# Kernel optimization log

Measured on AMD Instinct MI355X. Metric: run time of the kernel, lower is better.

## Reference

```python
import jax, jax.numpy as jnp
import numpy as np

DIM = 1024
N_HEADS = 16
HEAD_DIM = DIM // N_HEADS


def setup_inputs() -> dict:
    key = jax.random.key(0)
    ks = jax.random.split(key, 5)
    scale = 1.0 / np.sqrt(DIM)
    x = jax.random.normal(ks[0], (2, 2048, DIM), dtype=jnp.float32)
    W_qkv = jax.random.normal(ks[1], (DIM, 3 * DIM), dtype=jnp.float32) * scale
    b_qkv = jax.random.normal(ks[2], (3 * DIM,), dtype=jnp.float32) * 0.01
    W_proj = jax.random.normal(ks[3], (DIM, DIM), dtype=jnp.float32) * scale
    b_proj = jax.random.normal(ks[4], (DIM,), dtype=jnp.float32) * 0.01
    return {"x": x, "W_qkv": W_qkv, "b_qkv": b_qkv, "W_proj": W_proj, "b_proj": b_proj}


def reference(x, W_qkv, b_qkv, W_proj, b_proj):
    B, T, C = x.shape
    qkv = x @ W_qkv + b_qkv  # [B,T,3C]
    q, k, v = jnp.split(qkv, 3, axis=2)
    # [B,T,C] -> [B,H,T,Dh]
    def heads(y):
        return y.reshape(B, T, N_HEADS, HEAD_DIM).transpose(0, 2, 1, 3)
    q, k, v = heads(q), heads(k), heads(v)
    inv_sqrt_dh = 1.0 / jnp.sqrt(jnp.asarray(HEAD_DIM, dtype=x.dtype))
    attn = jnp.einsum('bhqd,bhkd->bhqk', q, k) * inv_sqrt_dh
    attn = jax.nn.softmax(attn, axis=-1)
    out = jnp.einsum('bhqk,bhkd->bhqd', attn, v)
    out = out.transpose(0, 2, 1, 3).reshape(B, T, C)
    return out @ W_proj + b_proj
```

## Files before the change

kernel.cpp:

```cpp
#include <hip/hip_runtime.h>
#include <hip/hip_bf16.h>
#include <math.h>

using bf16 = __hip_bfloat16;

typedef __bf16 bf16x8 __attribute__((ext_vector_type(8)));
typedef __bf16 bf16x4 __attribute__((ext_vector_type(4)));
typedef float  f32x4  __attribute__((ext_vector_type(4)));
typedef float  f32x16 __attribute__((ext_vector_type(16)));

constexpr int Bb = 2;
constexpr int Ts = 2048;
constexpr int Cc = 1024;
constexpr int Hh = 16;
constexpr int Dh = 64;
constexpr int Mm = Bb * Ts;
constexpr int Nqkv = 3 * Cc;
constexpr int BHTD = Bb * Hh * Ts * Dh;

__device__ __forceinline__
void gll16(const __bf16* g, __bf16* l)
{
    __builtin_amdgcn_global_load_lds(
        (const __attribute__((address_space(1))) unsigned int*)g,
        (__attribute__((address_space(3))) unsigned int*)l,
        16, 0, 0);
}

__global__ __launch_bounds__(256)
void prep_all(const float* __restrict__ x, __bf16* __restrict__ Xb,
              const float* __restrict__ Wq, __bf16* __restrict__ Wqt,
              const float* __restrict__ Wp, __bf16* __restrict__ Wpt)
{
    __shared__ __bf16 tl[64][72];
    const int bid = blockIdx.x;
    const int t = threadIdx.x;

    if (bid < 4096) {
        int i = (bid * 256 + t) * 4;
        float4 v = *(const float4*)(x + i);
        bf16x4 o = { (__bf16)v.x, (__bf16)v.y, (__bf16)v.z, (__bf16)v.w };
        *(bf16x4*)(Xb + i) = o;
        return;
    }
    const float* W; __bf16* Wt; int cols, bx, by;
    if (bid < 4096 + 768) {
        W = Wq; Wt = Wqt; cols = Nqkv;
        bx = (bid - 4096) % 48; by = (bid - 4096) / 48;
    } else {
        W = Wp; Wt = Wpt; cols = Cc;
        bx = (bid - 4864) % 16; by = (bid - 4864) / 16;
    }
    const int c0 = bx * 64;
    const int r0 = by * 64;
    #pragma unroll
    for (int i = 0; i < 4; i++) {
        int e = t + 256 * i;
        int r = e >> 4, c4 = (e & 15) * 4;
        float4 v = *(const float4*)(W + (r0 + r) * cols + c0 + c4);
        bf16x4 o = { (__bf16)v.x, (__bf16)v.y, (__bf16)v.z, (__bf16)v.w };
        *(bf16x4*)&tl[r][c4] = o;
    }
    __syncthreads();
    #pragma unroll
    for (int i = 0; i < 4; i++) {
        int e = t + 256 * i;
        int n = e >> 4, k4 = (e & 15) * 4;
        bf16x4 o = { tl[k4][n], tl[k4 + 1][n], tl[k4 + 2][n], tl[k4 + 3][n] };
        *(bf16x4*)(Wt + (c0 + n) * 1024 + r0 + k4) = o;
    }
}

template<int BM>
__device__ __forceinline__
void gemm_core(const __bf16* __restrict__ A, const __bf16* __restrict__ Bt,
               int m0, int n0, int wm, int wn, int quad, int l16, int t,
               f32x4 (&acc)[4][4])
{
    __shared__ __bf16 Al[BM][32];
    __shared__ __bf16 Bl[128][32];

    constexpr int MT = BM / 32;
    const int wave = t >> 6;
    const int lane = t & 63;
    const int srow = lane >> 2;
    const int scol = (lane & 3) * 8;

    const __bf16* Ag = A  + (size_t)(m0 + wave * 16 + srow) * 1024 + scol;
    const __bf16* Bg = Bt + (size_t)(n0 + wave * 16 + srow) * 1024 + scol;
    __bf16* Al_lo = &Al[wave * 16][0];
    __bf16* Bl_lo = &Bl[wave * 16][0];
    __bf16* Bl_hi = &Bl[64 + wave * 16][0];

    for (int k0 = 0; k0 < 1024; k0 += 32) {
        gll16(Ag + k0, Al_lo);
        if constexpr (BM == 128) {
            __bf16* Al_hi = &Al[64 + wave * 16][0];
            gll16(Ag + k0 + 64 * 1024, Al_hi);
        }
        gll16(Bg + k0,             Bl_lo);
        gll16(Bg + k0 + 64 * 1024, Bl_hi);
        __syncthreads();
        bf16x8 af[MT], bfr[4];
        #pragma unroll
        for (int mt = 0; mt < MT; mt++)
            af[mt] = *(const bf16x8*)&Al[wm * (BM / 2) + mt * 16 + l16][quad * 8];
        #pragma unroll
        for (int nt = 0; nt < 4; nt++)
            bfr[nt] = *(const bf16x8*)&Bl[wn * 64 + nt * 16 + l16][quad * 8];
        #pragma unroll
        for (int mt = 0; mt < MT; mt++)
            #pragma unroll
            for (int nt = 0; nt < 4; nt++)
                acc[mt][nt] = __builtin_amdgcn_mfma_f32_16x16x32_bf16(
                    af[mt], bfr[nt], acc[mt][nt], 0, 0, 0);
        __syncthreads();
    }
}

__global__ __launch_bounds__(256)
void qkv_mfma(const __bf16* __restrict__ A, const __bf16* __restrict__ Bt,
              const float* __restrict__ bias, __bf16* __restrict__ qkv)
{
    __shared__ __bf16 ebuf[4][64][72];

    const int t    = threadIdx.x;
    const int wave = t >> 6;
    const int lane = t & 63;
    const int quad = lane >> 4;
    const int l16  = lane & 15;
    const int wm   = wave >> 1, wn = wave & 1;
    const int n0 = blockIdx.x * 128;
    const int m0 = blockIdx.y * 128;

    f32x4 acc[4][4];
    #pragma unroll
    for (int i = 0; i < 4; i++)
        #pragma unroll
        for (int j = 0; j < 4; j++)
            acc[i][j] = f32x4{0.f, 0.f, 0.f, 0.f};

    gemm_core<128>(A, Bt, m0, n0, wm, wn, quad, l16, t, acc);

    const int nw0 = n0 + wn * 64;
    const int which = nw0 >> 10;
    const int h = (nw0 & 1023) >> 6;

    if (which == 2) {
        #pragma unroll
        for (int nt = 0; nt < 4; nt++) {
            int d = nt * 16 + l16;
            float bs = bias[nw0 + nt * 16 + l16];
            #pragma unroll
            for (int mt = 0; mt < 4; mt++) {
                int m = m0 + wm * 64 + mt * 16 + quad * 4;
                int b = m >> 11;
                int tt = m & 2047;
                bf16x4 o = { (__bf16)(acc[mt][nt][0] + bs),
                             (__bf16)(acc[mt][nt][1] + bs),
                             (__bf16)(acc[mt][nt][2] + bs),
                             (__bf16)(acc[mt][nt][3] + bs) };
                *(bf16x4*)&qkv[2 * (size_t)BHTD +
                               (((size_t)(b * 16 + h) * 64 + d) * 2048 + tt)] = o;
            }
        }
    } else {
        #pragma unroll
        for (int nt = 0; nt < 4; nt++) {
            float bs = bias[nw0 + nt * 16 + l16];
            #pragma unroll
            for (int mt = 0; mt < 4; mt++)
                #pragma unroll
                for (int r = 0; r < 4; r++)
                    ebuf[wave][mt * 16 + quad * 4 + r][nt * 16 + l16] =
                        (__bf16)(acc[mt][nt][r] + bs);
        }
        int m = m0 + wm * 64 + lane;
        int b = m >> 11;
        int tt = m & 2047;
        __bf16* dst = &qkv[which * (size_t)BHTD +
                           (((size_t)(b * 16 + h) * 2048 + tt) * 64)];
        #pragma unroll
        for (int c = 0; c < 8; c++)
            *(bf16x8*)(dst + c * 8) = *(const bf16x8*)&ebuf[wave][lane][c * 8];
    }
}

__global__ __launch_bounds__(256)
void proj_mfma(const __bf16* __restrict__ A, const __bf16* __restrict__ Bt,
               const float* __restrict__ bias, float* __restrict__ out)
{
    const int t    = threadIdx.x;
    const int wave = t >> 6;
    const int lane = t & 63;
    const int quad = lane >> 4;
    const int l16  = lane & 15;
    const int wm   = wave >> 1, wn = wave & 1;
    const int n0 = blockIdx.x * 128;
    const int m0 = blockIdx.y * 64;

    f32x4 acc[4][4];
    #pragma unroll
    for (int i = 0; i < 4; i++)
        #pragma unroll
        for (int j = 0; j < 4; j++)
            acc[i][j] = f32x4{0.f, 0.f, 0.f, 0.f};

    gemm_core<64>(A, Bt, m0, n0, wm, wn, quad, l16, t, acc);

    #pragma unroll
    for (int nt = 0; nt < 4; nt++) {
        int n = n0 + wn * 64 + nt * 16 + l16;
        float bs = bias[n];
        #pragma unroll
        for (int mt = 0; mt < 2; mt++) {
            #pragma unroll
            for (int r = 0; r < 4; r++) {
                int m = m0 + wm * 32 + mt * 16 + quad * 4 + r;
                out[m * 1024 + n] = acc[mt][nt][r] + bs;
            }
        }
    }
}

__global__ __launch_bounds__(512, 2)
void attn_mfma(const __bf16* __restrict__ Q, const __bf16* __restrict__ K,
               const __bf16* __restrict__ VT, __bf16* __restrict__ O)
{
    __shared__ __bf16 sK[2][3][64 * 64];
    __shared__ __bf16 sV[2][3][64 * 64];
    __shared__ float  slsum[4][2][64];

    const int t    = threadIdx.x;
    const int wave = t >> 6;
    const int lane = t & 63;
    const int qg   = wave & 3;
    const int kh   = wave >> 2;
    const int c    = lane & 31;
    const int hi   = lane >> 5;
    const int hx   = hi * 16;
    const int sw   = (c & 7) << 4;

    const int blk = blockIdx.x;
    const int bh  = blk & 31;
    const int qc  = blk >> 5;
    const int q0  = qc * 256 + qg * 64;

    const __bf16* Qp = Q  + ((size_t)bh * Ts + q0) * Dh;
    const __bf16* Kp = K  + (size_t)bh * Ts * Dh;
    const __bf16* Vp = VT + (size_t)bh * Dh * Ts;

    const float qscale = 0.125f * 1.44269504088896f;
    bf16x8 qf[2][4];
    #pragma unroll
    for (int qs = 0; qs < 2; qs++)
        #pragma unroll
        for (int ds = 0; ds < 4; ds++) {
            bf16x8 v = *(const bf16x8*)(Qp + (qs * 32 + c) * Dh + ds * 16 + hi * 8);
            #pragma unroll
            for (int i = 0; i < 8; i++) v[i] = (__bf16)(qscale * (float)v[i]);
            qf[qs][ds] = v;
        }

    f32x16 accO[2][2];
    #pragma unroll
    for (int qs = 0; qs < 2; qs++)
        #pragma unroll
        for (int dt = 0; dt < 2; dt++)
            #pragma unroll
            for (int i = 0; i < 16; i++) accO[qs][dt][i] = 0.f;
    float lsum[2] = {0.f, 0.f};

    const f32x16 z16 = {0.f, 0.f, 0.f, 0.f, 0.f, 0.f, 0.f, 0.f,
                        0.f, 0.f, 0.f, 0.f, 0.f, 0.f, 0.f, 0.f};

    const int r0 = qg * 8 + (lane >> 3);
    const int s8 = ((lane & 7) ^ (r0 & 7)) * 8;
    const __bf16* kg0 = Kp + (size_t)(kh * 1024 + r0) * Dh + s8;
    const __bf16* kg1 = kg0 + 32 * Dh;
    const __bf16* vg0 = Vp + (size_t)r0 * Ts + kh * 1024 + s8;
    const __bf16* vg1 = vg0 + (size_t)32 * Ts;

    gll16(kg0, &sK[kh][0][qg * 512]);
    gll16(kg1, &sK[kh][0][2048 + qg * 512]);
    gll16(vg0, &sV[kh][0][qg * 512]);
    gll16(vg1, &sV[kh][0][2048 + qg * 512]);

    for (int j = 0; j < 16; j++) {
        const int p = j % 3;
        if (j < 15) {
            const int pn = (j + 1) % 3;
            gll16(kg0 + (j + 1) * 4096, &sK[kh][pn][qg * 512]);
            gll16(kg1 + (j + 1) * 4096, &sK[kh][pn][2048 + qg * 512]);
            gll16(vg0 + (j + 1) * 64,   &sV[kh][pn][qg * 512]);
            gll16(vg1 + (j + 1) * 64,   &sV[kh][pn][2048 + qg * 512]);
            asm volatile("s_waitcnt vmcnt(4)" ::: "memory");
        } else {
            asm volatile("s_waitcnt vmcnt(0)" ::: "memory");
        }
        __builtin_amdgcn_s_barrier();
        __builtin_amdgcn_sched_barrier(0);

        const char* kb = (const char*)&sK[kh][p][0];
        const char* vb = (const char*)&sV[kh][p][0];

        bf16x8 kf[2][4];
        #pragma unroll
        for (int kt = 0; kt < 2; kt++) {
            const char* rbase = kb + (kt * 32 + c) * 128;
            #pragma unroll
            for (int ds = 0; ds < 4; ds++)
                kf[kt][ds] = *(const bf16x8*)(rbase + ((ds * 32 + hx) ^ sw));
        }

        f32x16 st[2][2];
        __builtin_amdgcn_s_setprio(1);
        #pragma unroll
        for (int kt = 0; kt < 2; kt++)
            #pragma unroll
            for (int qs = 0; qs < 2; qs++)
                st[qs][kt] = __builtin_amdgcn_mfma_f32_32x32x16_bf16(
                    kf[kt][0], qf[qs][0], z16, 0, 0, 0);
        #pragma unroll
        for (int ds = 1; ds < 4; ds++)
            #pragma unroll
            for (int kt = 0; kt < 2; kt++)
                #pragma unroll
                for (int qs = 0; qs < 2; qs++)
                    st[qs][kt] = __builtin_amdgcn_mfma_f32_32x32x16_bf16(
                        kf[kt][ds], qf[qs][ds], st[qs][kt], 0, 0, 0);
        __builtin_amdgcn_s_setprio(0);

        bf16x8 pa[2][4];
        #pragma unroll
        for (int qs = 0; qs < 2; qs++) {
            unsigned pk[2][8];
            #pragma unroll
            for (int kt = 0; kt < 2; kt++) {
                float sum0 = 0.f, sum1 = 0.f;
                #pragma unroll
                for (int r = 0; r < 16; r++) {
                    float pv = __builtin_amdgcn_exp2f(st[qs][kt][r]);
                    st[qs][kt][r] = pv;
                    if (r & 1) sum1 += pv; else sum0 += pv;
                }
                lsum[qs] += sum0 + sum1;
                #pragma unroll
                for (int r2 = 0; r2 < 8; r2++) {
                    unsigned d;
                    asm("v_cvt_pk_bf16_f32 %0, %1, %2"
                        : "=v"(d)
                        : "v"(st[qs][kt][2 * r2]), "v"(st[qs][kt][2 * r2 + 1]));
                    pk[kt][r2] = d;
                }
            }
            #pragma unroll
            for (int s = 0; s < 4; s++) {
                const int kt = s >> 1, r4 = (s & 1) * 4;
                unsigned x0 = pk[kt][r4 + 0], y0 = pk[kt][r4 + 2];
                unsigned x1 = pk[kt][r4 + 1], y1 = pk[kt][r4 + 3];
                asm("v_permlane32_swap_b32 %0, %1" : "+v"(x0), "+v"(y0));
                asm("v_permlane32_swap_b32 %0, %1" : "+v"(x1), "+v"(y1));
                union { unsigned u[4]; bf16x8 b; } pu;
                pu.u[0] = x0; pu.u[1] = x1; pu.u[2] = y0; pu.u[3] = y1;
                pa[qs][s] = pu.b;
            }
        }

        __builtin_amdgcn_s_setprio(1);
        #pragma unroll
        for (int s = 0; s < 4; s++)
            #pragma unroll
            for (int dt = 0; dt < 2; dt++) {
                bf16x8 vf = *(const bf16x8*)(vb + (dt * 32 + c) * 128 +
                                             ((s * 32 + hx) ^ sw));
                #pragma unroll
                for (int qs = 0; qs < 2; qs++)
                    accO[qs][dt] = __builtin_amdgcn_mfma_f32_32x32x16_bf16(
                        pa[qs][s], vf, accO[qs][dt], 0, 0, 0);
            }
        __builtin_amdgcn_s_setprio(0);
    }

    __syncthreads();

    float* pb = (qg < 2) ? (float*)&sK[0][0][0] + qg * 4096
                         : (float*)&sV[0][0][0] + (qg - 2) * 4096;
    if (kh == 1) {
        #pragma unroll
        for (int qs = 0; qs < 2; qs++) {
            #pragma unroll
            for (int dt = 0; dt < 2; dt++)
                #pragma unroll
                for (int r = 0; r < 16; r++)
                    pb[((qs * 2 + dt) << 10) + (r << 6) + lane] = accO[qs][dt][r];
            slsum[qg][qs][lane] = lsum[qs];
        }
    }
    __syncthreads();
    if (kh == 0) {
        #pragma unroll
        for (int qs = 0; qs < 2; qs++) {
            #pragma unroll
            for (int dt = 0; dt < 2; dt++)
                #pragma unroll
                for (int r = 0; r < 16; r++)
                    accO[qs][dt][r] += pb[((qs * 2 + dt) << 10) + (r << 6) + lane];
            lsum[qs] += slsum[qg][qs][lane];
        }

        const int b = bh >> 4, h = bh & 15;
        #pragma unroll
        for (int qs = 0; qs < 2; qs++) {
            float l = lsum[qs] + __shfl_xor(lsum[qs], 32);
            float linv = 1.f / l;
            #pragma unroll
            for (int r = 0; r < 16; r++) {
                const int qrow = (r & 3) + 8 * (r >> 2) + 4 * hi;
                float inv = __shfl(linv, qrow);
                __bf16* Op = O + ((size_t)(b * Ts + q0 + qs * 32 + qrow)) * Cc +
                             h * 64 + c;
                Op[0]  = (__bf16)(accO[qs][0][r] * inv);
                Op[32] = (__bf16)(accO[qs][1][r] * inv);
            }
        }
    }
}

extern "C" void kernel_launch(void* const* d_in, const int* in_sizes, int n_in,
                              void* d_out, int out_size, void* d_ws, size_t ws_size,
                              hipStream_t stream)
{
    (void)in_sizes; (void)n_in; (void)out_size; (void)ws_size;
    const float* x     = (const float*)d_in[0];
    const float* Wqkv  = (const float*)d_in[1];
    const float* bqkv  = (const float*)d_in[2];
    const float* Wproj = (const float*)d_in[3];
    const float* bproj = (const float*)d_in[4];
    float* out = (float*)d_out;

    __bf16* ws   = (__bf16*)d_ws;
    __bf16* Qw   = ws;
    __bf16* XbAO = ws + 3 * (size_t)BHTD;
    __bf16* Wqt  = XbAO + (size_t)Mm * Cc;
    __bf16* Wpt  = Wqt + (size_t)Nqkv * Cc;

    prep_all<<<dim3(5120), 256, 0, stream>>>(x, XbAO, Wqkv, Wqt, Wproj, Wpt);
    qkv_mfma<<<dim3(Nqkv / 128, Mm / 128), 256, 0, stream>>>(XbAO, Wqt, bqkv, Qw);
    attn_mfma<<<dim3(256), 512, 0, stream>>>(
        Qw, Qw + BHTD, Qw + 2 * (size_t)BHTD, XbAO);
    proj_mfma<<<dim3(Cc / 128, Mm / 64), 256, 0, stream>>>(XbAO, Wpt, bproj, out);
}
```

Measured before the change: 179.9 us.

## Fuse attention and output projection into one cooperative kernel with grid sync

Merges the attention kernel and the output projection GEMM into a single cooperative launch, separated by a grid-wide barrier. After the sync, each 512-thread block runs two 256-thread projection tiles, reusing the attention shared memory for the GEMM staging buffers. The aim is to remove one kernel launch and the gap between the two kernels. In exchange it adds grid-sync overhead and a cooperative-launch requirement, and falls back to the two separate launches if the cooperative launch fails.

```diff
diff --git a/kernel.cpp b/kernel.cpp
--- a/kernel.cpp
+++ b/kernel.cpp
@@ -1,6 +1,9 @@
 #include <hip/hip_runtime.h>
 #include <hip/hip_bf16.h>
+#include <hip/hip_cooperative_groups.h>
 #include <math.h>
+
+namespace cg = cooperative_groups;
 
 using bf16 = __hip_bfloat16;
 
@@ -97,6 +100,50 @@
         if constexpr (BM == 128) {
             __bf16* Al_hi = &Al[64 + wave * 16][0];
             gll16(Ag + k0 + 64 * 1024, Al_hi);
+        }
+        gll16(Bg + k0,             Bl_lo);
+        gll16(Bg + k0 + 64 * 1024, Bl_hi);
+        __syncthreads();
+        bf16x8 af[MT], bfr[4];
+        #pragma unroll
+        for (int mt = 0; mt < MT; mt++)
+            af[mt] = *(const bf16x8*)&Al[wm * (BM / 2) + mt * 16 + l16][quad * 8];
+        #pragma unroll
+        for (int nt = 0; nt < 4; nt++)
+            bfr[nt] = *(const bf16x8*)&Bl[wn * 64 + nt * 16 + l16][quad * 8];
+        #pragma unroll
+        for (int mt = 0; mt < MT; mt++)
+            #pragma unroll
+            for (int nt = 0; nt < 4; nt++)
+                acc[mt][nt] = __builtin_amdgcn_mfma_f32_16x16x32_bf16(
+                    af[mt], bfr[nt], acc[mt][nt], 0, 0, 0);
+        __syncthreads();
+    }
+}
+
+template<int BM>
+__device__ __forceinline__
+void gemm_core_p(__bf16 (*Al)[32], __bf16 (*Bl)[32],
+                 const __bf16* __restrict__ A, const __bf16* __restrict__ Bt,
+                 int m0, int n0, int wm, int wn, int quad, int l16, int th,
+                 f32x4 (&acc)[4][4])
+{
+    constexpr int MT = BM / 32;
+    const int wave = th >> 6;
+    const int lane = th & 63;
+    const int srow = lane >> 2;
+    const int scol = (lane & 3) * 8;
+
+    const __bf16* Ag = A  + (size_t)(m0 + wave * 16 + srow) * 1024 + scol;
+    const __bf16* Bg = Bt + (size_t)(n0 + wave * 16 + srow) * 1024 + scol;
+    __bf16* Al_lo = &Al[wave * 16][0];
+    __bf16* Bl_lo = &Bl[wave * 16][0];
+    __bf16* Bl_hi = &Bl[64 + wave * 16][0];
+
+    for (int k0 = 0; k0 < 1024; k0 += 32) {
+        gll16(Ag + k0, Al_lo);
+        if constexpr (BM == 128) {
+            gll16(Ag + k0 + 64 * 1024, &Al[64 + wave * 16][0]);
         }
         gll16(Bg + k0,             Bl_lo);
         gll16(Bg + k0 + 64 * 1024, Bl_hi);
@@ -223,14 +270,12 @@
     }
 }
 
-__global__ __launch_bounds__(512, 2)
-void attn_mfma(const __bf16* __restrict__ Q, const __bf16* __restrict__ K,
-               const __bf16* __restrict__ VT, __bf16* __restrict__ O)
-{
-    __shared__ __bf16 sK[2][3][64 * 64];
-    __shared__ __bf16 sV[2][3][64 * 64];
-    __shared__ float  slsum[4][2][64];
-
+__device__ __forceinline__
+void attn_body(const __bf16* __restrict__ Q, const __bf16* __restrict__ K,
+               const __bf16* __restrict__ VT, __bf16* __restrict__ O,
+               __bf16 (*sK)[3][64 * 64], __bf16 (*sV)[3][64 * 64],
+               float (*slsum)[2][64])
+{
     const int t    = threadIdx.x;
     const int wave = t >> 6;
     const int lane = t & 63;
@@ -427,6 +472,71 @@
     }
 }
 
+__global__ __launch_bounds__(512, 2)
+void attn_mfma(const __bf16* __restrict__ Q, const __bf16* __restrict__ K,
+               const __bf16* __restrict__ VT, __bf16* __restrict__ O)
+{
+    __shared__ __bf16 sK[2][3][64 * 64];
+    __shared__ __bf16 sV[2][3][64 * 64];
+    __shared__ float  slsum[4][2][64];
+    attn_body(Q, K, VT, O, sK, sV, slsum);
+}
+
+__global__ __launch_bounds__(512, 2)
+void attn_proj(const __bf16* __restrict__ Q, const __bf16* __restrict__ K,
+               const __bf16* __restrict__ VT, __bf16* __restrict__ AO,
+               const __bf16* __restrict__ Wpt, const float* __restrict__ bias,
+               float* __restrict__ out)
+{
+    __shared__ __bf16 sK[2][3][64 * 64];
+    __shared__ __bf16 sV[2][3][64 * 64];
+    __shared__ float  slsum[4][2][64];
+
+    attn_body(Q, K, VT, AO, sK, sV, slsum);
+
+    __threadfence();
+    cg::this_grid().sync();
+
+    const int t    = threadIdx.x;
+    const int half = t >> 8;
+    const int th   = t & 255;
+    const int wv   = th >> 6;
+    const int ln   = th & 63;
+    const int qd   = ln >> 4;
+    const int l16p = ln & 15;
+    const int wm   = wv >> 1, wn = wv & 1;
+    const int vb = blockIdx.x * 2 + half;
+    const int n0 = (vb & 7) * 128;
+    const int m0 = (vb >> 3) * 64;
+
+    char* gb = (char*)&sK[0][0][0] + half * 12288;
+    __bf16 (*Al)[32] = (__bf16(*)[32])gb;
+    __bf16 (*Bl)[32] = (__bf16(*)[32])(gb + 4096);
+
+    f32x4 acc[4][4];
+    #pragma unroll
+    for (int i = 0; i < 4; i++)
+        #pragma unroll
+        for (int j2 = 0; j2 < 4; j2++)
+            acc[i][j2] = f32x4{0.f, 0.f, 0.f, 0.f};
+
+    gemm_core_p<64>(Al, Bl, AO, Wpt, m0, n0, wm, wn, qd, l16p, th, acc);
+
+    #pragma unroll
+    for (int nt = 0; nt < 4; nt++) {
+        int n = n0 + wn * 64 + nt * 16 + l16p;
+        float bs = bias[n];
+        #pragma unroll
+        for (int mt = 0; mt < 2; mt++) {
+            #pragma unroll
+            for (int r = 0; r < 4; r++) {
+                int m = m0 + wm * 32 + mt * 16 + qd * 4 + r;
+                out[m * 1024 + n] = acc[mt][nt][r] + bs;
+            }
+        }
+    }
+}
+
 extern "C" void kernel_launch(void* const* d_in, const int* in_sizes, int n_in,
                               void* d_out, int out_size, void* d_ws, size_t ws_size,
                               hipStream_t stream)
@@ -447,7 +557,17 @@
 
     prep_all<<<dim3(5120), 256, 0, stream>>>(x, XbAO, Wqkv, Wqt, Wproj, Wpt);
     qkv_mfma<<<dim3(Nqkv / 128, Mm / 128), 256, 0, stream>>>(XbAO, Wqt, bqkv, Qw);
-    attn_mfma<<<dim3(256), 512, 0, stream>>>(
-        Qw, Qw + BHTD, Qw + 2 * (size_t)BHTD, XbAO);
-    proj_mfma<<<dim3(Cc / 128, Mm / 64), 256, 0, stream>>>(XbAO, Wpt, bproj, out);
-}
+
+    const __bf16* Qc = Qw;
+    const __bf16* Kc = Qw + BHTD;
+    const __bf16* Vc = Qw + 2 * (size_t)BHTD;
+    __bf16* AO = XbAO;
+    void* a2[7] = { (void*)&Qc, (void*)&Kc, (void*)&Vc, (void*)&AO,
+                    (void*)&Wpt, (void*)&bproj, (void*)&out };
+    hipError_t e = hipLaunchCooperativeKernel((const void*)attn_proj,
+                                              dim3(256), dim3(512), a2, 0, stream);
+    if (e != hipSuccess) {
+        attn_mfma<<<dim3(256), 512, 0, stream>>>(Qc, Kc, Vc, AO);
+        proj_mfma<<<dim3(Cc / 128, Mm / 64), 256, 0, stream>>>(AO, Wpt, bproj, out);
+    }
+}
```

New measurement: 291.0 us. +61.8%, slower.

## Double GEMM K-tile to 64 with XOR-swizzled LDS and XCD-aware block remap

Applied to the files above, without the earlier changes.

The QKV and projection GEMM cores now stage a K-step of 64 instead of 32, which halves the number of barrier pairs per tile. The LDS layout uses an XOR swizzle of 16-byte chunks to avoid bank conflicts on the fragment reads. Block indices are remapped so that consecutive blocks on the same XCD cover neighbouring tiles, which should improve L2 reuse. The QKV kernel also aliases its epilogue buffer onto the GEMM shared memory, so LDS use stays bounded despite the larger tiles.

```diff
diff --git a/kernel.cpp b/kernel.cpp
--- a/kernel.cpp
+++ b/kernel.cpp
@@ -73,47 +73,47 @@
 
 template<int BM>
 __device__ __forceinline__
-void gemm_core(const __bf16* __restrict__ A, const __bf16* __restrict__ Bt,
-               int m0, int n0, int wm, int wn, int quad, int l16, int t,
-               f32x4 (&acc)[4][4])
-{
-    __shared__ __bf16 Al[BM][32];
-    __shared__ __bf16 Bl[128][32];
-
+void gemm_core64(__bf16 (*Al)[64], __bf16 (*Bl)[64],
+                 const __bf16* __restrict__ A, const __bf16* __restrict__ Bt,
+                 int m0, int n0, int wm, int wn, int quad, int l16, int t,
+                 f32x4 (&acc)[4][4])
+{
     constexpr int MT = BM / 32;
     const int wave = t >> 6;
     const int lane = t & 63;
-    const int srow = lane >> 2;
-    const int scol = (lane & 3) * 8;
-
-    const __bf16* Ag = A  + (size_t)(m0 + wave * 16 + srow) * 1024 + scol;
-    const __bf16* Bg = Bt + (size_t)(n0 + wave * 16 + srow) * 1024 + scol;
-    __bf16* Al_lo = &Al[wave * 16][0];
-    __bf16* Bl_lo = &Bl[wave * 16][0];
-    __bf16* Bl_hi = &Bl[64 + wave * 16][0];
-
-    for (int k0 = 0; k0 < 1024; k0 += 32) {
-        gll16(Ag + k0, Al_lo);
-        if constexpr (BM == 128) {
-            __bf16* Al_hi = &Al[64 + wave * 16][0];
-            gll16(Ag + k0 + 64 * 1024, Al_hi);
-        }
-        gll16(Bg + k0,             Bl_lo);
-        gll16(Bg + k0 + 64 * 1024, Bl_hi);
+    const int srow = lane >> 3;
+    const int scol = ((lane & 7) ^ srow) * 8;
+
+    const __bf16* Ag = A  + (size_t)(m0 + wave * (BM / 4) + srow) * 1024 + scol;
+    const __bf16* Bg = Bt + (size_t)(n0 + wave * 32 + srow) * 1024 + scol;
+
+    const int swz = (l16 & 7) << 4;
+
+    for (int k0 = 0; k0 < 1024; k0 += 64) {
+        #pragma unroll
+        for (int g = 0; g < BM / 32; g++)
+            gll16(Ag + k0 + (size_t)g * 8 * 1024, &Al[wave * (BM / 4) + g * 8][0]);
+        #pragma unroll
+        for (int g = 0; g < 4; g++)
+            gll16(Bg + k0 + (size_t)g * 8 * 1024, &Bl[wave * 32 + g * 8][0]);
         __syncthreads();
-        bf16x8 af[MT], bfr[4];
-        #pragma unroll
-        for (int mt = 0; mt < MT; mt++)
-            af[mt] = *(const bf16x8*)&Al[wm * (BM / 2) + mt * 16 + l16][quad * 8];
-        #pragma unroll
-        for (int nt = 0; nt < 4; nt++)
-            bfr[nt] = *(const bf16x8*)&Bl[wn * 64 + nt * 16 + l16][quad * 8];
-        #pragma unroll
-        for (int mt = 0; mt < MT; mt++)
+        #pragma unroll
+        for (int ks = 0; ks < 2; ks++) {
+            const int cb = (ks * 64 + quad * 16) ^ swz;
+            bf16x8 af[MT], bfr[4];
+            #pragma unroll
+            for (int mt = 0; mt < MT; mt++)
+                af[mt] = *(const bf16x8*)((const char*)&Al[wm * (BM / 2) + mt * 16 + l16][0] + cb);
             #pragma unroll
             for (int nt = 0; nt < 4; nt++)
-                acc[mt][nt] = __builtin_amdgcn_mfma_f32_16x16x32_bf16(
-                    af[mt], bfr[nt], acc[mt][nt], 0, 0, 0);
+                bfr[nt] = *(const bf16x8*)((const char*)&Bl[wn * 64 + nt * 16 + l16][0] + cb);
+            #pragma unroll
+            for (int mt = 0; mt < MT; mt++)
+                #pragma unroll
+                for (int nt = 0; nt < 4; nt++)
+                    acc[mt][nt] = __builtin_amdgcn_mfma_f32_16x16x32_bf16(
+                        af[mt], bfr[nt], acc[mt][nt], 0, 0, 0);
+        }
         __syncthreads();
     }
 }
@@ -122,7 +122,11 @@
 void qkv_mfma(const __bf16* __restrict__ A, const __bf16* __restrict__ Bt,
               const float* __restrict__ bias, __bf16* __restrict__ qkv)
 {
-    __shared__ __bf16 ebuf[4][64][72];
+    __shared__ __align__(16) char smem[36864];
+    __bf16 (*Al)[64] = (__bf16(*)[64])smem;
+    __bf16 (*Bl)[64] = (__bf16(*)[64])(smem + 16384);
+    typedef __bf16 (*ebuf_p)[64][72];
+    ebuf_p ebuf = (ebuf_p)smem;
 
     const int t    = threadIdx.x;
     const int wave = t >> 6;
@@ -130,8 +134,10 @@
     const int quad = lane >> 4;
     const int l16  = lane & 15;
     const int wm   = wave >> 1, wn = wave & 1;
-    const int n0 = blockIdx.x * 128;
-    const int m0 = blockIdx.y * 128;
+    const int bid  = blockIdx.x;
+    const int swb  = (bid & 7) * 96 + (bid >> 3);
+    const int n0 = (swb % 24) * 128;
+    const int m0 = (swb / 24) * 128;
 
     f32x4 acc[4][4];
     #pragma unroll
@@ -140,7 +146,7 @@
         for (int j = 0; j < 4; j++)
             acc[i][j] = f32x4{0.f, 0.f, 0.f, 0.f};
 
-    gemm_core<128>(A, Bt, m0, n0, wm, wn, quad, l16, t, acc);
+    gemm_core64<128>(Al, Bl, A, Bt, m0, n0, wm, wn, quad, l16, t, acc);
 
     const int nw0 = n0 + wn * 64;
     const int which = nw0 >> 10;
@@ -190,14 +196,19 @@
 void proj_mfma(const __bf16* __restrict__ A, const __bf16* __restrict__ Bt,
                const float* __restrict__ bias, float* __restrict__ out)
 {
+    __shared__ __bf16 Al[64][64];
+    __shared__ __bf16 Bl[128][64];
+
     const int t    = threadIdx.x;
     const int wave = t >> 6;
     const int lane = t & 63;
     const int quad = lane >> 4;
     const int l16  = lane & 15;
     const int wm   = wave >> 1, wn = wave & 1;
-    const int n0 = blockIdx.x * 128;
-    const int m0 = blockIdx.y * 64;
+    const int bid  = blockIdx.x;
+    const int swb  = (bid & 7) * 64 + (bid >> 3);
+    const int n0 = (swb & 7) * 128;
+    const int m0 = (swb >> 3) * 64;
 
     f32x4 acc[4][4];
     #pragma unroll
@@ -206,7 +217,7 @@
         for (int j = 0; j < 4; j++)
             acc[i][j] = f32x4{0.f, 0.f, 0.f, 0.f};
 
-    gemm_core<64>(A, Bt, m0, n0, wm, wn, quad, l16, t, acc);
+    gemm_core64<64>(Al, Bl, A, Bt, m0, n0, wm, wn, quad, l16, t, acc);
 
     #pragma unroll
     for (int nt = 0; nt < 4; nt++) {
@@ -446,8 +457,8 @@
     __bf16* Wpt  = Wqt + (size_t)Nqkv * Cc;
 
     prep_all<<<dim3(5120), 256, 0, stream>>>(x, XbAO, Wqkv, Wqt, Wproj, Wpt);
-    qkv_mfma<<<dim3(Nqkv / 128, Mm / 128), 256, 0, stream>>>(XbAO, Wqt, bqkv, Qw);
+    qkv_mfma<<<dim3(768), 256, 0, stream>>>(XbAO, Wqt, bqkv, Qw);
     attn_mfma<<<dim3(256), 512, 0, stream>>>(
         Qw, Qw + BHTD, Qw + 2 * (size_t)BHTD, XbAO);
-    proj_mfma<<<dim3(Cc / 128, Mm / 64), 256, 0, stream>>>(XbAO, Wpt, bproj, out);
-}
+    proj_mfma<<<dim3(512), 256, 0, stream>>>(XbAO, Wpt, bproj, out);
+}
```

Result: no change. 181.5 us (+0.9%).
